# Performance work log

Hardware: AMD Instinct MI355X
Metric: run time of the kernel (lower is better)

## Reference

```python
import jax, jax.numpy as jnp
import numpy as np

B, M, D, P, T = 512, 16, 128, 16, 4096
GAMMA = 1.0  # similarity_size


def setup_inputs() -> dict:
    key = jax.random.key(0)
    k1, k2, k3, k4, k5 = jax.random.split(key, 5)
    phi = jax.random.normal(k1, (B, P), dtype=jnp.float32)
    state = jax.random.normal(k2, (B, D), dtype=jnp.float32)
    trajectories = jax.random.normal(k3, (T, D), dtype=jnp.float32)
    # Stand-in per-model KAARMA state-transition parameters (linear recurrent + input map, tanh)
    A = jax.random.normal(k4, (M, D, D), dtype=jnp.float32) * (1.0 / np.sqrt(D))
    B_in = jax.random.normal(k5, (M, P, D), dtype=jnp.float32) * (1.0 / np.sqrt(P))
    return {"phi": phi, "state": state, "trajectories": trajectories, "A": A, "B_in": B_in}


def reference(phi, state, trajectories, A, B_in):
    # per-model state update: new_state[b,m,:] = tanh(state @ A_m + phi @ B_m)
    new_state = jnp.tanh(
        jnp.einsum("bd,mdh->bmh", state, A) + jnp.einsum("bp,mph->bmh", phi, B_in)
    )  # [B, M, D]
    # RBF similarity vs trajectory set via ||s||^2 + ||t||^2 - 2 s.t (single batched GEMM)
    s_sq = jnp.sum(new_state * new_state, axis=-1, keepdims=True)      # [B, M, 1]
    t_sq = jnp.sum(trajectories * trajectories, axis=-1)               # [T]
    cross = jnp.einsum("bmd,td->bmt", new_state, trajectories)         # [B, M, T]
    sq_dist = jnp.maximum(s_sq + t_sq[None, None, :] - 2.0 * cross, 0.0)
    sim = jnp.exp(-GAMMA * sq_dist)                                    # [B, M, T]
    output = sim.reshape(phi.shape[0], -1)                             # [B, M*T]
    return output, new_state
```

## Files before the change

### kernel.cpp

```cpp
#include <hip/hip_runtime.h>
#include <hip/hip_bf16.h>
#include <cstdint>
#include <cstddef>

#define NB 512
#define NM 16
#define ND 128
#define NP 16
#define NT 4096

typedef __bf16 bf16x8 __attribute__((ext_vector_type(8)));
typedef __bf16 bf16x4 __attribute__((ext_vector_type(4)));
typedef float f32x4 __attribute__((ext_vector_type(4)));

static_assert(sizeof(bf16x8) == 16, "bf16x8 must be 16B");

__global__ __launch_bounds__(256) void prep_kernel(
    const float* __restrict__ phi, const float* __restrict__ state,
    const float* __restrict__ traj, const float* __restrict__ A,
    const float* __restrict__ Bin, float* __restrict__ ns_out,
    __bf16* __restrict__ ns_bf, __bf16* __restrict__ tj_bf,
    float* __restrict__ s_sq, float* __restrict__ t_sq) {
  __shared__ alignas(16) float sSt[16 * 128];
  __shared__ alignas(16) float sPhi[16 * 16];
  __shared__ alignas(16) float sRes[16 * 128];
  const int tid = threadIdx.x;
  const int bx = blockIdx.x;

  if (bx < 512) {
    const int m = bx & 15;
    const int b0 = (bx >> 4) * 16;
    const float4* S4 = (const float4*)(state + (size_t)b0 * 128);
    float4* sSt4 = (float4*)sSt;
    sSt4[tid] = S4[tid];
    sSt4[tid + 256] = S4[tid + 256];
    sPhi[tid] = phi[b0 * 16 + tid];
    __syncthreads();

    const int h2 = tid & 63;
    const int rgrp = tid >> 6;
    const float* Ap = A + (size_t)m * 16384 + h2;
    const float* Bp = Bin + (size_t)m * 2048 + h2;

    float acc[2][4];
#pragma unroll
    for (int hi = 0; hi < 2; ++hi)
#pragma unroll
      for (int j = 0; j < 4; ++j) acc[hi][j] = 0.f;

#pragma unroll 4
    for (int c = 0; c < 32; ++c) {
      float a0[4], a1[4];
#pragma unroll
      for (int u = 0; u < 4; ++u) {
        a0[u] = Ap[(size_t)(c * 4 + u) * 128];
        a1[u] = Ap[(size_t)(c * 4 + u) * 128 + 64];
      }
#pragma unroll
      for (int j = 0; j < 4; ++j) {
        const f32x4 sv = *(const f32x4*)&sSt[(rgrp * 4 + j) * 128 + c * 4];
#pragma unroll
        for (int u = 0; u < 4; ++u) {
          acc[0][j] = fmaf(sv[u], a0[u], acc[0][j]);
          acc[1][j] = fmaf(sv[u], a1[u], acc[1][j]);
        }
      }
    }
#pragma unroll
    for (int pc = 0; pc < 4; ++pc) {
      float b0v[4], b1v[4];
#pragma unroll
      for (int u = 0; u < 4; ++u) {
        b0v[u] = Bp[(size_t)(pc * 4 + u) * 128];
        b1v[u] = Bp[(size_t)(pc * 4 + u) * 128 + 64];
      }
#pragma unroll
      for (int j = 0; j < 4; ++j) {
        const f32x4 pv = *(const f32x4*)&sPhi[(rgrp * 4 + j) * 16 + pc * 4];
#pragma unroll
        for (int u = 0; u < 4; ++u) {
          acc[0][j] = fmaf(pv[u], b0v[u], acc[0][j]);
          acc[1][j] = fmaf(pv[u], b1v[u], acc[1][j]);
        }
      }
    }

#pragma unroll
    for (int j = 0; j < 4; ++j) {
      const int row = rgrp * 4 + j;
      const int R = (b0 + row) * 16 + m;
      const float v0 = tanhf(acc[0][j]);
      const float v1 = tanhf(acc[1][j]);
      ns_out[(size_t)R * 128 + h2] = v0;
      ns_out[(size_t)R * 128 + h2 + 64] = v1;
      sRes[row * 128 + h2] = v0;
      sRes[row * 128 + h2 + 64] = v1;
      float s = v0 * v0 + v1 * v1;
#pragma unroll
      for (int o = 32; o > 0; o >>= 1) s += __shfl_xor(s, o);
      if (h2 == 0) s_sq[R] = s;
    }
    __syncthreads();

    {
      const int row = tid >> 4;
      const int kb = tid & 15;
      const f32x4 r0 = *(const f32x4*)&sRes[row * 128 + kb * 8];
      const f32x4 r1 = *(const f32x4*)&sRes[row * 128 + kb * 8 + 4];
      bf16x8 o;
#pragma unroll
      for (int i = 0; i < 4; ++i) {
        o[i] = (__bf16)r0[i];
        o[i + 4] = (__bf16)r1[i];
      }
      const int R = (b0 + row) * 16 + m;
      *(bf16x8*)(ns_bf + (size_t)R * 128 + kb * 8) = o;
    }
  } else {
    const int t0 = (bx - 512) * 128;
    const int t = t0 + (tid >> 1);
    const int half = tid & 1;
    float s = 0.f;
#pragma unroll
    for (int q = 0; q < 8; ++q) {
      const int kb = half * 8 + q;
      const f32x4 v0 = *(const f32x4*)&traj[(size_t)t * 128 + kb * 8];
      const f32x4 v1 = *(const f32x4*)&traj[(size_t)t * 128 + kb * 8 + 4];
      s += v0[0] * v0[0] + v0[1] * v0[1] + v0[2] * v0[2] + v0[3] * v0[3];
      s += v1[0] * v1[0] + v1[1] * v1[1] + v1[2] * v1[2] + v1[3] * v1[3];
      bf16x8 o;
#pragma unroll
      for (int i = 0; i < 4; ++i) {
        o[i] = (__bf16)v0[i];
        o[i + 4] = (__bf16)v1[i];
      }
      *(bf16x8*)(tj_bf + (size_t)t * 128 + kb * 8) = o;
    }
    s += __shfl_xor(s, 1);
    if (half == 0) t_sq[t] = s;
  }
}

__global__ __launch_bounds__(256, 3) void sim_kernel(
    const __bf16* __restrict__ ns_bf, const __bf16* __restrict__ tj_bf,
    const float* __restrict__ s_sq, const float* __restrict__ t_sq,
    float* __restrict__ out) {
  const int tid = threadIdx.x;
  const int lane = tid & 63;
  const int w = tid >> 6;
  const int R0 = blockIdx.x * 128;
  const int C0 = blockIdx.y * 128;
  const int rbase = (w >> 1) * 64;
  const int cbase = (w & 1) * 64;
  const int l15 = lane & 15;
  const int quad = lane >> 4;

  const __bf16* Ap = ns_bf + (size_t)(R0 + rbase + l15) * 128 + quad * 8;
  const __bf16* Bp = tj_bf + (size_t)(C0 + cbase + l15) * 128 + quad * 8;

  f32x4 acc[4][4];
#pragma unroll
  for (int i = 0; i < 4; ++i)
#pragma unroll
    for (int j = 0; j < 4; ++j) acc[i][j] = (f32x4){0.f, 0.f, 0.f, 0.f};

#pragma unroll
  for (int ks = 0; ks < 4; ++ks) {
    bf16x8 af[4], bfr[4];
#pragma unroll
    for (int i = 0; i < 4; ++i)
      af[i] = *(const bf16x8*)(Ap + i * 2048 + ks * 32);
#pragma unroll
    for (int i = 0; i < 4; ++i)
      bfr[i] = *(const bf16x8*)(Bp + i * 2048 + ks * 32);
#pragma unroll
    for (int ri = 0; ri < 4; ++ri)
#pragma unroll
      for (int ci = 0; ci < 4; ++ci)
        acc[ri][ci] = __builtin_amdgcn_mfma_f32_16x16x32_bf16(
            bfr[ci], af[ri], acc[ri][ci], 0, 0, 0);
  }

  f32x4 tq[4];
#pragma unroll
  for (int ci = 0; ci < 4; ++ci)
    tq[ci] = *(const f32x4*)&t_sq[C0 + cbase + ci * 16 + quad * 4];
#pragma unroll
  for (int ri = 0; ri < 4; ++ri) {
    const int nsrow = rbase + ri * 16 + l15;
    const float sq = s_sq[R0 + nsrow];
    float* orow = out + (size_t)(R0 + nsrow) * NT + C0;
#pragma unroll
    for (int ci = 0; ci < 4; ++ci) {
      const int t4 = cbase + ci * 16 + quad * 4;
      f32x4 r;
#pragma unroll
      for (int k = 0; k < 4; ++k) {
        const float d = fmaxf(sq + tq[ci][k] - 2.f * acc[ri][ci][k], 0.f);
        r[k] = __expf(-d);
      }
      *(f32x4*)&orow[t4] = r;
    }
  }
}

extern "C" void kernel_launch(void* const* d_in, const int* in_sizes, int n_in,
                              void* d_out, int out_size, void* d_ws,
                              size_t ws_size, hipStream_t stream) {
  (void)in_sizes; (void)n_in; (void)out_size; (void)ws_size;
  const float* phi   = (const float*)d_in[0];
  const float* state = (const float*)d_in[1];
  const float* traj  = (const float*)d_in[2];
  const float* A     = (const float*)d_in[3];
  const float* Bin   = (const float*)d_in[4];

  float* out = (float*)d_out;
  float* out_ns = out + (size_t)NB * NM * NT;

  char* ws = (char*)d_ws;
  __bf16* ns_bf = (__bf16*)ws;
  __bf16* tj_bf = (__bf16*)(ws + (2u << 20));
  float* s_sq   = (float*)(ws + (3u << 20));
  float* t_sq   = (float*)(ws + (3u << 20) + (32u << 10));

  prep_kernel<<<544, 256, 0, stream>>>(phi, state, traj, A, Bin, out_ns, ns_bf,
                                       tj_bf, s_sq, t_sq);
  dim3 g2(NB * NM / 128, NT / 128);
  sim_kernel<<<g2, 256, 0, stream>>>(ns_bf, tj_bf, s_sq, t_sq, out);
}
```

Baseline: 183.9 us.

## Stage similarity GEMM tiles in LDS with async double-buffered loads and swizzle

The similarity kernel becomes a 256-block grid. Each block keeps one 128-row state tile resident in LDS and loops over 8 trajectory column tiles. Trajectory tiles are brought in with global_load_lds into a double buffer, so the next tile loads while the current one is computed and its exp epilogue is stored. The prep kernel now writes the bf16 copies with an XOR-swizzled 16-byte chunk order so the LDS fragment reads avoid bank conflicts. The aim is to cut repeated global/L2 fragment loads, at the cost of one block per CU with 96KB of LDS and less latency hiding for the large output stores.

```diff
diff --git a/kernel.cpp b/kernel.cpp
--- a/kernel.cpp
+++ b/kernel.cpp
@@ -10,10 +10,15 @@
 #define NT 4096
 
 typedef __bf16 bf16x8 __attribute__((ext_vector_type(8)));
-typedef __bf16 bf16x4 __attribute__((ext_vector_type(4)));
 typedef float f32x4 __attribute__((ext_vector_type(4)));
 
 static_assert(sizeof(bf16x8) == 16, "bf16x8 must be 16B");
+
+__device__ __forceinline__ void gload_lds16(const void* g, void* l) {
+  __builtin_amdgcn_global_load_lds(
+      (const __attribute__((address_space(1))) unsigned int*)g,
+      (__attribute__((address_space(3))) unsigned int*)l, 16, 0, 0);
+}
 
 __global__ __launch_bounds__(256) void prep_kernel(
     const float* __restrict__ phi, const float* __restrict__ state,
@@ -114,7 +119,7 @@
         o[i + 4] = (__bf16)r1[i];
       }
       const int R = (b0 + row) * 16 + m;
-      *(bf16x8*)(ns_bf + (size_t)R * 128 + kb * 8) = o;
+      *(bf16x8*)(ns_bf + (size_t)R * 128 + ((kb ^ m) * 8)) = o;
     }
   } else {
     const int t0 = (bx - 512) * 128;
@@ -134,73 +139,108 @@
         o[i] = (__bf16)v0[i];
         o[i + 4] = (__bf16)v1[i];
       }
-      *(bf16x8*)(tj_bf + (size_t)t * 128 + kb * 8) = o;
+      *(bf16x8*)(tj_bf + (size_t)t * 128 + ((kb ^ (t & 15)) * 8)) = o;
     }
     s += __shfl_xor(s, 1);
     if (half == 0) t_sq[t] = s;
   }
 }
 
-__global__ __launch_bounds__(256, 3) void sim_kernel(
+__global__ __launch_bounds__(256, 1) void sim_kernel(
     const __bf16* __restrict__ ns_bf, const __bf16* __restrict__ tj_bf,
     const float* __restrict__ s_sq, const float* __restrict__ t_sq,
     float* __restrict__ out) {
+  __shared__ alignas(16) __bf16 sNS[128 * 128];
+  __shared__ alignas(16) __bf16 sT[2][128 * 128];
   const int tid = threadIdx.x;
   const int lane = tid & 63;
   const int w = tid >> 6;
-  const int R0 = blockIdx.x * 128;
-  const int C0 = blockIdx.y * 128;
+  const int p = blockIdx.x;
+  const int R0 = (p >> 2) * 128;
+  const int Cg = (p & 3) * 8;
   const int rbase = (w >> 1) * 64;
   const int cbase = (w & 1) * 64;
   const int l15 = lane & 15;
   const int quad = lane >> 4;
 
-  const __bf16* Ap = ns_bf + (size_t)(R0 + rbase + l15) * 128 + quad * 8;
-  const __bf16* Bp = tj_bf + (size_t)(C0 + cbase + l15) * 128 + quad * 8;
-
-  f32x4 acc[4][4];
-#pragma unroll
-  for (int i = 0; i < 4; ++i)
-#pragma unroll
-    for (int j = 0; j < 4; ++j) acc[i][j] = (f32x4){0.f, 0.f, 0.f, 0.f};
-
-#pragma unroll
-  for (int ks = 0; ks < 4; ++ks) {
-    bf16x8 af[4], bfr[4];
+  const char* gNS = (const char*)(ns_bf + (size_t)R0 * 128);
+  const char* gT0 = (const char*)(tj_bf + (size_t)(Cg * 128) * 128);
+#pragma unroll
+  for (int it = 0; it < 8; ++it) {
+    const int off = it * 4096 + w * 1024;
+    gload_lds16(gNS + off + lane * 16, (char*)sNS + off);
+    gload_lds16(gT0 + off + lane * 16, (char*)sT[0] + off);
+  }
+  __syncthreads();
+
+  bf16x8 af[4][4];
+#pragma unroll
+  for (int ks = 0; ks < 4; ++ks)
 #pragma unroll
     for (int i = 0; i < 4; ++i)
-      af[i] = *(const bf16x8*)(Ap + i * 2048 + ks * 32);
+      af[ks][i] = *(const bf16x8*)&sNS[(rbase + i * 16 + l15) * 128 +
+                                       (((quad + ks * 4) ^ l15) * 8)];
+  float sqr[4];
+#pragma unroll
+  for (int ri = 0; ri < 4; ++ri)
+    sqr[ri] = s_sq[R0 + rbase + ri * 16 + l15];
+
+#pragma unroll
+  for (int t = 0; t < 8; ++t) {
+    const int cur = t & 1;
+    if (t + 1 < 8) {
+      const char* gT = (const char*)(tj_bf + (size_t)((Cg + t + 1) * 128) * 128);
+#pragma unroll
+      for (int it = 0; it < 8; ++it) {
+        const int off = it * 4096 + w * 1024;
+        gload_lds16(gT + off + lane * 16, (char*)sT[cur ^ 1] + off);
+      }
+    }
+
+    f32x4 acc[4][4];
 #pragma unroll
     for (int i = 0; i < 4; ++i)
-      bfr[i] = *(const bf16x8*)(Bp + i * 2048 + ks * 32);
-#pragma unroll
-    for (int ri = 0; ri < 4; ++ri)
-#pragma unroll
-      for (int ci = 0; ci < 4; ++ci)
-        acc[ri][ci] = __builtin_amdgcn_mfma_f32_16x16x32_bf16(
-            bfr[ci], af[ri], acc[ri][ci], 0, 0, 0);
-  }
-
-  f32x4 tq[4];
-#pragma unroll
-  for (int ci = 0; ci < 4; ++ci)
-    tq[ci] = *(const f32x4*)&t_sq[C0 + cbase + ci * 16 + quad * 4];
-#pragma unroll
-  for (int ri = 0; ri < 4; ++ri) {
-    const int nsrow = rbase + ri * 16 + l15;
-    const float sq = s_sq[R0 + nsrow];
-    float* orow = out + (size_t)(R0 + nsrow) * NT + C0;
-#pragma unroll
-    for (int ci = 0; ci < 4; ++ci) {
-      const int t4 = cbase + ci * 16 + quad * 4;
-      f32x4 r;
-#pragma unroll
-      for (int k = 0; k < 4; ++k) {
-        const float d = fmaxf(sq + tq[ci][k] - 2.f * acc[ri][ci][k], 0.f);
-        r[k] = __expf(-d);
-      }
-      *(f32x4*)&orow[t4] = r;
-    }
+#pragma unroll
+      for (int j = 0; j < 4; ++j) acc[i][j] = (f32x4){0.f, 0.f, 0.f, 0.f};
+
+    const __bf16* sB = sT[cur];
+#pragma unroll
+    for (int ks = 0; ks < 4; ++ks) {
+      bf16x8 bfr[4];
+#pragma unroll
+      for (int i = 0; i < 4; ++i)
+        bfr[i] = *(const bf16x8*)&sB[(cbase + i * 16 + l15) * 128 +
+                                     (((quad + ks * 4) ^ l15) * 8)];
+#pragma unroll
+      for (int ri = 0; ri < 4; ++ri)
+#pragma unroll
+        for (int ci = 0; ci < 4; ++ci)
+          acc[ri][ci] = __builtin_amdgcn_mfma_f32_16x16x32_bf16(
+              bfr[ci], af[ks][ri], acc[ri][ci], 0, 0, 0);
+    }
+
+    const int C0 = (Cg + t) * 128;
+    f32x4 tq[4];
+#pragma unroll
+    for (int ci = 0; ci < 4; ++ci)
+      tq[ci] = *(const f32x4*)&t_sq[C0 + cbase + ci * 16 + quad * 4];
+#pragma unroll
+    for (int ri = 0; ri < 4; ++ri) {
+      const float sq = sqr[ri];
+      float* orow = out + (size_t)(R0 + rbase + ri * 16 + l15) * NT + C0;
+#pragma unroll
+      for (int ci = 0; ci < 4; ++ci) {
+        const int t4 = cbase + ci * 16 + quad * 4;
+        f32x4 r;
+#pragma unroll
+        for (int k = 0; k < 4; ++k) {
+          const float d = fmaxf(sq + tq[ci][k] - 2.f * acc[ri][ci][k], 0.f);
+          r[k] = __expf(-d);
+        }
+        *(f32x4*)&orow[t4] = r;
+      }
+    }
+    __syncthreads();
   }
 }
 
@@ -225,6 +265,5 @@
 
   prep_kernel<<<544, 256, 0, stream>>>(phi, state, traj, A, Bin, out_ns, ns_bf,
                                        tj_bf, s_sq, t_sq);
-  dim3 g2(NB * NM / 128, NT / 128);
-  sim_kernel<<<g2, 256, 0, stream>>>(ns_bf, tj_bf, s_sq, t_sq, out);
-}
+  sim_kernel<<<256, 256, 0, stream>>>(ns_bf, tj_bf, s_sq, t_sq, out);
+}
```

Result: faster. 175.0 us (-4.8%).
